# Performance work log

Measured on AMD Instinct MI355X. Metric: run time of the kernel, lower is better.

## Reference

```python
import jax, jax.numpy as jnp
import numpy as np

MAX_DISTANCE = 50.0


def setup_inputs() -> dict:
    key = jax.random.key(0)
    ks = jax.random.split(key, 12)
    B, N, D = 32, 64, 256
    ID = 128  # interaction_dim
    IN = 2 * D + 4  # 516
    H = 2 * ID  # 256
    s = lambda fan_in: 1.0 / np.sqrt(fan_in)
    return {
        "slots": jax.random.normal(ks[0], (B, N, D), jnp.float32),
        "positions": jax.random.normal(ks[1], (B, N, 4), jnp.float32),
        "existence_mask": jnp.ones((B, N), jnp.float32),
        "W1": jax.random.uniform(ks[2], (IN, H), jnp.float32, -s(IN), s(IN)),
        "b1": jax.random.uniform(ks[3], (H,), jnp.float32, -s(IN), s(IN)),
        "W2": jax.random.uniform(ks[4], (H, ID), jnp.float32, -s(H), s(H)),
        "b2": jax.random.uniform(ks[5], (ID,), jnp.float32, -s(H), s(H)),
        "Wt": jax.random.uniform(ks[6], (ID, 8), jnp.float32, -s(ID), s(ID)),
        "bt": jax.random.uniform(ks[7], (8,), jnp.float32, -s(ID), s(ID)),
        "Wc": jax.random.uniform(ks[8], (ID, 1), jnp.float32, -s(ID), s(ID)),
        "bc": jax.random.uniform(ks[9], (1,), jnp.float32, -s(ID), s(ID)),
    }


def reference(slots, positions, existence_mask, W1, b1, W2, b2, Wt, bt, Wc, bc):
    B, N, D = slots.shape
    # all-pairs broadcast of slots: [B, N, N, D]
    slots_i = jnp.broadcast_to(slots[:, :, None, :], (B, N, N, D))
    slots_j = jnp.broadcast_to(slots[:, None, :, :], (B, N, N, D))
    # relative xy position and distance  [B, N, N, 2] / [B, N, N, 1]
    rel_pos = positions[:, :, None, :2] - positions[:, None, :, :2]
    d2 = jnp.sum(rel_pos * rel_pos, axis=-1, keepdims=True)
    safe = jnp.where(d2 == 0, 1.0, d2)
    distance = jnp.where(d2 == 0, 0.0, jnp.sqrt(safe))  # zero-safe norm (matches torch subgradient)
    dn = distance / MAX_DISTANCE
    pair = jnp.concatenate(
        [slots_i, slots_j, rel_pos, dn, jnp.minimum(dn, 1.0)], axis=-1
    )  # [B, N, N, 2D+4]
    h = jax.nn.relu(jnp.einsum("bijf,fh->bijh", pair, W1) + b1)
    feats = jnp.einsum("bijh,hd->bijd", h, W2) + b2  # [B, N, N, ID]
    mask = existence_mask[:, :, None] * existence_mask[:, None, :]  # [B, N, N]
    feats = feats * mask[..., None]
    itypes = jnp.einsum("bijd,dk->bijk", feats, Wt) + bt  # [B, N, N, 8]
    causal = jax.nn.sigmoid(
        (jnp.einsum("bijd,dk->bijk", feats, Wc) + bc)[..., 0]
    ) * mask  # [B, N, N]
    return feats, itypes, causal
```

## Files before the change

kernel.cpp:

```cpp
#include <hip/hip_runtime.h>
#include <hip/hip_bf16.h>
#include <math.h>


typedef __attribute__((ext_vector_type(8))) short  bfrag8;
typedef __attribute__((ext_vector_type(4))) short  spack4;
typedef __attribute__((ext_vector_type(4))) float  fvec4;

#define ITY_OFF   16777216u
#define CAU_OFF   17825792u

static __device__ __forceinline__ short f2bf(float f) {
  unsigned u = __float_as_uint(f);
  u = u + 0x7FFF + ((u >> 16) & 1);
  return (short)(u >> 16);
}
static __device__ __forceinline__ float bf2f(short s) {
  return __uint_as_float(((unsigned)(unsigned short)s) << 16);
}

__global__ __launch_bounds__(256) void prep_wtx(
    const float* __restrict__ W2,
    const float* __restrict__ b2,
    const float* __restrict__ Wt,
    const float* __restrict__ Wc,
    float* __restrict__ Wtx,
    float* __restrict__ b2e)
{
  __shared__ float colv[128];
  __shared__ float red[4];
  const int q   = blockIdx.x;
  const int tid = threadIdx.x;
  if (tid < 128) colv[tid] = (q < 8) ? Wt[tid * 8 + q] : Wc[tid];
  __syncthreads();

  float acc = 0.f;
  #pragma unroll 4
  for (int c = 0; c < 128; ++c)
    acc = fmaf(W2[tid * 128 + c], colv[c], acc);
  Wtx[tid * 16 + q] = acc;

  float p = (tid < 128) ? b2[tid] * colv[tid] : 0.f;
  #pragma unroll
  for (int m = 1; m < 64; m <<= 1) p += __shfl_xor(p, m, 64);
  if ((tid & 63) == 0) red[tid >> 6] = p;
  __syncthreads();
  if (tid == 0) b2e[128 + q] = red[0] + red[1] + red[2] + red[3];
  if (q == 0) {
    if (tid < 128) b2e[tid] = b2[tid];
    if (tid >= 137 && tid < 144) b2e[tid] = 0.f;
  }
}

__global__ __launch_bounds__(256) void prep_w(
    const float* __restrict__ W2,
    const float* __restrict__ Wtx,
    short* __restrict__ WfHi,
    short* __restrict__ WfLo)
{
  const int tid  = threadIdx.x;
  const int tile = blockIdx.x * 4 + (tid >> 6);
  const int l    = tid & 63;
  const int ks   = tile / 9, db = tile - ks * 9;
  const int d    = db * 16 + (l & 15);
  const int k0   = ks * 32 + ((l >> 4) & 3) * 8;

  float v[8];
  if (d < 128) {
    #pragma unroll
    for (int e = 0; e < 8; ++e) v[e] = W2[(k0 + e) * 128 + d];
  } else if (d < 137) {
    #pragma unroll
    for (int e = 0; e < 8; ++e) v[e] = Wtx[(k0 + e) * 16 + (d - 128)];
  } else {
    #pragma unroll
    for (int e = 0; e < 8; ++e) v[e] = 0.f;
  }

  bfrag8 hi, lo;
  #pragma unroll
  for (int e = 0; e < 8; ++e) {
    const short hb = f2bf(v[e]);
    hi[e] = hb;
    lo[e] = f2bf(v[e] - bf2f(hb));
  }
  *(bfrag8*)&WfHi[(tile * 64 + l) * 8] = hi;
  *(bfrag8*)&WfLo[(tile * 64 + l) * 8] = lo;
}

__global__ __launch_bounds__(512) void prep_ac(
    const float* __restrict__ slots,
    const float* __restrict__ W1,
    const float* __restrict__ b1,
    float* __restrict__ Abuf,
    float* __restrict__ Cbuf)
{
  __shared__ __align__(16) float s[4][256];
  __shared__ float pA[4][256], pC[4][256];
  const int tid  = threadIdx.x;
  const int col  = tid & 255;
  const int kh   = tid >> 8;
  const int row0 = blockIdx.x * 4;
  {
    const int r = tid >> 7, o = (tid & 127) * 2;
    *(float2*)&s[r][o] = *(const float2*)&slots[(row0 + r) * 256 + o];
  }
  __syncthreads();

  float aA[4] = {0.f,0.f,0.f,0.f};
  float aC[4] = {0.f,0.f,0.f,0.f};
  const int kbase = kh * 128;
  #pragma unroll 2
  for (int kk = 0; kk < 128; ++kk) {
    const int k = kbase + kk;
    const float wa = W1[k * 256 + col];
    const float wc = W1[(256 + k) * 256 + col];
    #pragma unroll
    for (int r = 0; r < 4; ++r) {
      aA[r] = fmaf(s[r][k], wa, aA[r]);
      aC[r] = fmaf(s[r][k], wc, aC[r]);
    }
  }
  if (kh == 1) {
    #pragma unroll
    for (int r = 0; r < 4; ++r) { pA[r][col] = aA[r]; pC[r][col] = aC[r]; }
  }
  __syncthreads();
  if (kh == 0) {
    const float bv = b1[col];
    #pragma unroll
    for (int r = 0; r < 4; ++r) {
      Abuf[(row0 + r) * 256 + col] = aA[r] + pA[r][col] + bv;
      Cbuf[(row0 + r) * 256 + col] = aC[r] + pC[r][col];
    }
  }
}

__global__ __launch_bounds__(256, 4) void main_kernel(
    const float* __restrict__ positions,
    const float* __restrict__ em,
    const float* __restrict__ W1,
    const float* __restrict__ Abuf,
    const float* __restrict__ Cbuf,
    const float* __restrict__ b2e,
    const short* __restrict__ WfHi,
    const short* __restrict__ WfLo,
    const float* __restrict__ bt,
    const float* __restrict__ bc,
    float* __restrict__ out)
{
  __shared__ __align__(16) char LDSbuf[32768];
  __shared__ float maskL[32];

  const int tid = threadIdx.x;
  const int l   = tid & 63;
  const int w   = tid >> 6;
  const int wid   = (blockIdx.x & 7) * 512 + (blockIdx.x >> 3);
  const int b     = wid >> 7;
  const int i     = (wid >> 1) & 63;
  const int jhalf = wid & 1;
  const int rowi  = b * 64 + i;
  const int j0    = jhalf * 32;

  if (tid < 32) maskL[tid] = em[rowi] * em[b * 64 + j0 + tid];

  char* HhiB = LDSbuf;
  char* HloB = LDSbuf + 16384;

  {
    const int jsub = l >> 4;
    const int kl4  = (l & 15) * 4;
    const float pxi = positions[rowi * 4 + 0];
    const float pyi = positions[rowi * 4 + 1];
    float grx[2], gry[2], gdn[2], gdc[2];
    #pragma unroll
    for (int jj = 0; jj < 2; ++jj) {
      const int rowj = b * 64 + j0 + w * 8 + jsub * 2 + jj;
      const float rx = pxi - positions[rowj * 4 + 0];
      const float ry = pyi - positions[rowj * 4 + 1];
      const float d2 = rx * rx + ry * ry;
      const float dist = (d2 == 0.f) ? 0.f : sqrtf(d2);
      const float dn = dist * (1.0f / 50.0f);
      grx[jj] = rx; gry[jj] = ry; gdn[jj] = dn; gdc[jj] = fminf(dn, 1.f);
    }
    #pragma unroll 1
    for (int kb = 0; kb < 4; ++kb) {
      const int k = kb * 64 + kl4;
      const fvec4 a4 = *(const fvec4*)&Abuf[rowi * 256 + k];
      const fvec4 g0 = *(const fvec4*)&W1[512 * 256 + k];
      const fvec4 g1 = *(const fvec4*)&W1[513 * 256 + k];
      const fvec4 g2 = *(const fvec4*)&W1[514 * 256 + k];
      const fvec4 g3 = *(const fvec4*)&W1[515 * 256 + k];
      #pragma unroll
      for (int jj = 0; jj < 2; ++jj) {
        const int j = w * 8 + jsub * 2 + jj;
        const fvec4 c4 = *(const fvec4*)&Cbuf[(b * 64 + j0 + j) * 256 + k];
        spack4 hi, lo;
        #pragma unroll
        for (int e = 0; e < 4; ++e) {
          float h = a4[e] + c4[e] + grx[jj] * g0[e] + gry[jj] * g1[e]
                  + gdn[jj] * g2[e] + gdc[jj] * g3[e];
          h = fmaxf(h, 0.f);
          const short hb = f2bf(h);
          hi[e] = hb;
          lo[e] = f2bf(h - bf2f(hb));
        }
        const int byte = (j * 512 + k * 2) ^ ((j & 7) << 4);
        *(spack4*)(HhiB + byte) = hi;
        *(spack4*)(HloB + byte) = lo;
      }
    }
  }
  __syncthreads();

  const int laneJ = l & 15;
  const int laneK = l >> 4;
  const int addrA = laneJ * 512 + laneK * 16;
  const int swzA  = (laneJ & 7) << 4;

  fvec4 acc[2][2];
  fvec4 acc8;
  acc[0][0] = 0.f; acc[0][1] = 0.f; acc[1][0] = 0.f; acc[1][1] = 0.f;
  acc8 = 0.f;

  const int db0 = 2 * w, db1 = 2 * w + 1;
  const bool has8 = (w >= 2);
  const int jb8 = w - 2;

  #pragma unroll
  for (int ks = 0; ks < 8; ++ks) {
    const bfrag8 bh0 = *(const bfrag8*)&WfHi[((ks * 9 + db0) * 64 + l) * 8];
    const bfrag8 bl0 = *(const bfrag8*)&WfLo[((ks * 9 + db0) * 64 + l) * 8];
    const bfrag8 bh1 = *(const bfrag8*)&WfHi[((ks * 9 + db1) * 64 + l) * 8];
    const bfrag8 bl1 = *(const bfrag8*)&WfLo[((ks * 9 + db1) * 64 + l) * 8];
    bfrag8 bh8 = {}, bl8 = {};
    if (has8) {
      bh8 = *(const bfrag8*)&WfHi[((ks * 9 + 8) * 64 + l) * 8];
      bl8 = *(const bfrag8*)&WfLo[((ks * 9 + 8) * 64 + l) * 8];
    }
    #pragma unroll
    for (int jb = 0; jb < 2; ++jb) {
      const int base = addrA + jb * 8192 + ks * 64;
      const bfrag8 ah = *(const bfrag8*)(HhiB + (base ^ swzA));
      const bfrag8 al = *(const bfrag8*)(HloB + (base ^ swzA));
      acc[jb][0] = __builtin_amdgcn_mfma_f32_16x16x32_bf16(ah, bh0, acc[jb][0], 0, 0, 0);
      acc[jb][0] = __builtin_amdgcn_mfma_f32_16x16x32_bf16(ah, bl0, acc[jb][0], 0, 0, 0);
      acc[jb][0] = __builtin_amdgcn_mfma_f32_16x16x32_bf16(al, bh0, acc[jb][0], 0, 0, 0);
      acc[jb][1] = __builtin_amdgcn_mfma_f32_16x16x32_bf16(ah, bh1, acc[jb][1], 0, 0, 0);
      acc[jb][1] = __builtin_amdgcn_mfma_f32_16x16x32_bf16(ah, bl1, acc[jb][1], 0, 0, 0);
      acc[jb][1] = __builtin_amdgcn_mfma_f32_16x16x32_bf16(al, bh1, acc[jb][1], 0, 0, 0);
      if (has8 && jb == jb8) {
        acc8 = __builtin_amdgcn_mfma_f32_16x16x32_bf16(ah, bh8, acc8, 0, 0, 0);
        acc8 = __builtin_amdgcn_mfma_f32_16x16x32_bf16(ah, bl8, acc8, 0, 0, 0);
        acc8 = __builtin_amdgcn_mfma_f32_16x16x32_bf16(al, bh8, acc8, 0, 0, 0);
      }
    }
  }

  __syncthreads();

  float* FS = (float*)LDSbuf;
  #pragma unroll
  for (int t = 0; t < 2; ++t) {
    const int d = (2 * w + t) * 16 + laneJ;
    const float bv = b2e[d];
    #pragma unroll
    for (int jb = 0; jb < 2; ++jb) {
      #pragma unroll
      for (int r = 0; r < 4; ++r) {
        const int j = jb * 16 + laneK * 4 + r;
        FS[j * 148 + d] = (acc[jb][t][r] + bv) * maskL[j];
      }
    }
  }
  if (has8) {
    const int d8 = 128 + laneJ;
    const float bv = b2e[d8];
    #pragma unroll
    for (int r = 0; r < 4; ++r) {
      const int j = jb8 * 16 + laneK * 4 + r;
      FS[j * 148 + d8] = (acc8[r] + bv) * maskL[j];
    }
  }
  __syncthreads();

  {
    const int j  = tid >> 3;
    const int dq = (tid & 7) * 16;
    const size_t orow = ((size_t)rowi * 64 + j0 + j) * 128;
    #pragma unroll
    for (int q = 0; q < 4; ++q) {
      const fvec4 v = *(const fvec4*)&FS[j * 148 + dq + q * 4];
      *(fvec4*)&out[orow + dq + q * 4] = v;
    }
    const int q8 = tid & 7;
    out[(size_t)ITY_OFF + ((size_t)rowi * 64 + j0 + j) * 8 + q8] =
        FS[j * 148 + 128 + q8] + bt[q8];
    if (tid < 32) {
      const float z = FS[tid * 148 + 136] + bc[0];
      out[(size_t)CAU_OFF + (size_t)rowi * 64 + j0 + tid] =
          maskL[tid] / (1.f + expf(-z));
    }
  }
}

extern "C" void kernel_launch(void* const* d_in, const int* in_sizes, int n_in,
                              void* d_out, int out_size, void* d_ws, size_t ws_size,
                              hipStream_t stream) {
  const float* slots     = (const float*)d_in[0];
  const float* positions = (const float*)d_in[1];
  const float* em        = (const float*)d_in[2];
  const float* W1        = (const float*)d_in[3];
  const float* b1        = (const float*)d_in[4];
  const float* W2        = (const float*)d_in[5];
  const float* b2        = (const float*)d_in[6];
  const float* Wt        = (const float*)d_in[7];
  const float* bt        = (const float*)d_in[8];
  const float* Wc        = (const float*)d_in[9];
  const float* bc        = (const float*)d_in[10];
  float* out = (float*)d_out;

  float* Abuf = (float*)d_ws;
  float* Cbuf = Abuf + 524288;
  float* b2e  = Cbuf + 524288;
  float* Wtx  = b2e + 256;
  short* WfHi = (short*)(Wtx + 4096);
  short* WfLo = WfHi + 36864;

  prep_wtx<<<9,   256, 0, stream>>>(W2, b2, Wt, Wc, Wtx, b2e);
  prep_w  <<<18,  256, 0, stream>>>(W2, Wtx, WfHi, WfLo);
  prep_ac <<<512, 512, 0, stream>>>(slots, W1, b1, Abuf, Cbuf);
  main_kernel<<<4096, 256, 0, stream>>>(positions, em, W1, Abuf, Cbuf,
                                        b2e, WfHi, WfLo, bt, bc, out);
}
```

Before: 173.3 us.

## Process four full i-rows per block with register-resident W2 fragments

Each block now covers a batch and a group of four i rows, with all 64 j values per row, instead of one half-row. The W2 MFMA B-fragments for each wave's two output tiles are loaded into registers once and reused across the four rows, and the grid shrinks from 4096 to 512 blocks. LDS doubles to 64 KB and the occupancy hint drops to 2 blocks per CU. The intent is to cut redundant weight loads and per-block overhead, at the cost of higher register pressure, serialized per-row phases, and fewer blocks to hide latency.

```diff
diff --git a/kernel.cpp b/kernel.cpp
--- a/kernel.cpp
+++ b/kernel.cpp
@@ -136,7 +136,7 @@
   }
 }
 
-__global__ __launch_bounds__(256, 4) void main_kernel(
+__global__ __launch_bounds__(256, 2) void main_kernel(
     const float* __restrict__ positions,
     const float* __restrict__ em,
     const float* __restrict__ W1,
@@ -149,158 +149,166 @@
     const float* __restrict__ bc,
     float* __restrict__ out)
 {
-  __shared__ __align__(16) char LDSbuf[32768];
-  __shared__ float maskL[32];
+  __shared__ __align__(16) char LDSbuf[65536];
+  __shared__ float maskL[64];
 
   const int tid = threadIdx.x;
   const int l   = tid & 63;
   const int w   = tid >> 6;
-  const int wid   = (blockIdx.x & 7) * 512 + (blockIdx.x >> 3);
-  const int b     = wid >> 7;
-  const int i     = (wid >> 1) & 63;
-  const int jhalf = wid & 1;
-  const int rowi  = b * 64 + i;
-  const int j0    = jhalf * 32;
-
-  if (tid < 32) maskL[tid] = em[rowi] * em[b * 64 + j0 + tid];
+  const int wid = (blockIdx.x & 7) * 64 + (blockIdx.x >> 3);
+  const int b   = wid >> 4;
+  const int ig  = wid & 15;
+
+  if (tid < 64) maskL[tid] = em[b * 64 + tid];
 
   char* HhiB = LDSbuf;
-  char* HloB = LDSbuf + 16384;
-
-  {
-    const int jsub = l >> 4;
-    const int kl4  = (l & 15) * 4;
-    const float pxi = positions[rowi * 4 + 0];
-    const float pyi = positions[rowi * 4 + 1];
-    float grx[2], gry[2], gdn[2], gdc[2];
-    #pragma unroll
-    for (int jj = 0; jj < 2; ++jj) {
-      const int rowj = b * 64 + j0 + w * 8 + jsub * 2 + jj;
-      const float rx = pxi - positions[rowj * 4 + 0];
-      const float ry = pyi - positions[rowj * 4 + 1];
-      const float d2 = rx * rx + ry * ry;
-      const float dist = (d2 == 0.f) ? 0.f : sqrtf(d2);
-      const float dn = dist * (1.0f / 50.0f);
-      grx[jj] = rx; gry[jj] = ry; gdn[jj] = dn; gdc[jj] = fminf(dn, 1.f);
-    }
-    #pragma unroll 1
-    for (int kb = 0; kb < 4; ++kb) {
-      const int k = kb * 64 + kl4;
-      const fvec4 a4 = *(const fvec4*)&Abuf[rowi * 256 + k];
-      const fvec4 g0 = *(const fvec4*)&W1[512 * 256 + k];
-      const fvec4 g1 = *(const fvec4*)&W1[513 * 256 + k];
-      const fvec4 g2 = *(const fvec4*)&W1[514 * 256 + k];
-      const fvec4 g3 = *(const fvec4*)&W1[515 * 256 + k];
-      #pragma unroll
-      for (int jj = 0; jj < 2; ++jj) {
-        const int j = w * 8 + jsub * 2 + jj;
-        const fvec4 c4 = *(const fvec4*)&Cbuf[(b * 64 + j0 + j) * 256 + k];
-        spack4 hi, lo;
-        #pragma unroll
-        for (int e = 0; e < 4; ++e) {
-          float h = a4[e] + c4[e] + grx[jj] * g0[e] + gry[jj] * g1[e]
-                  + gdn[jj] * g2[e] + gdc[jj] * g3[e];
-          h = fmaxf(h, 0.f);
-          const short hb = f2bf(h);
-          hi[e] = hb;
-          lo[e] = f2bf(h - bf2f(hb));
-        }
-        const int byte = (j * 512 + k * 2) ^ ((j & 7) << 4);
-        *(spack4*)(HhiB + byte) = hi;
-        *(spack4*)(HloB + byte) = lo;
-      }
-    }
-  }
-  __syncthreads();
+  char* HloB = LDSbuf + 32768;
+
+  bfrag8 rbh0[8], rbl0[8], rbh1[8], rbl1[8];
+  #pragma unroll
+  for (int ks = 0; ks < 8; ++ks) {
+    rbh0[ks] = *(const bfrag8*)&WfHi[((ks * 9 + 2 * w    ) * 64 + l) * 8];
+    rbl0[ks] = *(const bfrag8*)&WfLo[((ks * 9 + 2 * w    ) * 64 + l) * 8];
+    rbh1[ks] = *(const bfrag8*)&WfHi[((ks * 9 + 2 * w + 1) * 64 + l) * 8];
+    rbl1[ks] = *(const bfrag8*)&WfLo[((ks * 9 + 2 * w + 1) * 64 + l) * 8];
+  }
 
   const int laneJ = l & 15;
   const int laneK = l >> 4;
   const int addrA = laneJ * 512 + laneK * 16;
   const int swzA  = (laneJ & 7) << 4;
 
-  fvec4 acc[2][2];
-  fvec4 acc8;
-  acc[0][0] = 0.f; acc[0][1] = 0.f; acc[1][0] = 0.f; acc[1][1] = 0.f;
-  acc8 = 0.f;
-
-  const int db0 = 2 * w, db1 = 2 * w + 1;
-  const bool has8 = (w >= 2);
-  const int jb8 = w - 2;
-
-  #pragma unroll
-  for (int ks = 0; ks < 8; ++ks) {
-    const bfrag8 bh0 = *(const bfrag8*)&WfHi[((ks * 9 + db0) * 64 + l) * 8];
-    const bfrag8 bl0 = *(const bfrag8*)&WfLo[((ks * 9 + db0) * 64 + l) * 8];
-    const bfrag8 bh1 = *(const bfrag8*)&WfHi[((ks * 9 + db1) * 64 + l) * 8];
-    const bfrag8 bl1 = *(const bfrag8*)&WfLo[((ks * 9 + db1) * 64 + l) * 8];
-    bfrag8 bh8 = {}, bl8 = {};
-    if (has8) {
-      bh8 = *(const bfrag8*)&WfHi[((ks * 9 + 8) * 64 + l) * 8];
-      bl8 = *(const bfrag8*)&WfLo[((ks * 9 + 8) * 64 + l) * 8];
-    }
-    #pragma unroll
-    for (int jb = 0; jb < 2; ++jb) {
-      const int base = addrA + jb * 8192 + ks * 64;
-      const bfrag8 ah = *(const bfrag8*)(HhiB + (base ^ swzA));
-      const bfrag8 al = *(const bfrag8*)(HloB + (base ^ swzA));
-      acc[jb][0] = __builtin_amdgcn_mfma_f32_16x16x32_bf16(ah, bh0, acc[jb][0], 0, 0, 0);
-      acc[jb][0] = __builtin_amdgcn_mfma_f32_16x16x32_bf16(ah, bl0, acc[jb][0], 0, 0, 0);
-      acc[jb][0] = __builtin_amdgcn_mfma_f32_16x16x32_bf16(al, bh0, acc[jb][0], 0, 0, 0);
-      acc[jb][1] = __builtin_amdgcn_mfma_f32_16x16x32_bf16(ah, bh1, acc[jb][1], 0, 0, 0);
-      acc[jb][1] = __builtin_amdgcn_mfma_f32_16x16x32_bf16(ah, bl1, acc[jb][1], 0, 0, 0);
-      acc[jb][1] = __builtin_amdgcn_mfma_f32_16x16x32_bf16(al, bh1, acc[jb][1], 0, 0, 0);
-      if (has8 && jb == jb8) {
-        acc8 = __builtin_amdgcn_mfma_f32_16x16x32_bf16(ah, bh8, acc8, 0, 0, 0);
-        acc8 = __builtin_amdgcn_mfma_f32_16x16x32_bf16(ah, bl8, acc8, 0, 0, 0);
-        acc8 = __builtin_amdgcn_mfma_f32_16x16x32_bf16(al, bh8, acc8, 0, 0, 0);
-      }
-    }
-  }
-
-  __syncthreads();
-
-  float* FS = (float*)LDSbuf;
-  #pragma unroll
-  for (int t = 0; t < 2; ++t) {
-    const int d = (2 * w + t) * 16 + laneJ;
-    const float bv = b2e[d];
-    #pragma unroll
-    for (int jb = 0; jb < 2; ++jb) {
+  #pragma unroll 1
+  for (int ii = 0; ii < 4; ++ii) {
+    const int rowi = b * 64 + ig * 4 + ii;
+    const float emi = em[rowi];
+
+    {
+      const int jsub = laneK;
+      const float pxi = positions[rowi * 4 + 0];
+      const float pyi = positions[rowi * 4 + 1];
+      float grx[4], gry[4], gdn[4], gdc[4];
+      #pragma unroll
+      for (int jj = 0; jj < 4; ++jj) {
+        const int rowj = b * 64 + w * 16 + jsub * 4 + jj;
+        const float rx = pxi - positions[rowj * 4 + 0];
+        const float ry = pyi - positions[rowj * 4 + 1];
+        const float d2 = rx * rx + ry * ry;
+        const float dist = (d2 == 0.f) ? 0.f : sqrtf(d2);
+        const float dn = dist * (1.0f / 50.0f);
+        grx[jj] = rx; gry[jj] = ry; gdn[jj] = dn; gdc[jj] = fminf(dn, 1.f);
+      }
+      #pragma unroll 1
+      for (int kb = 0; kb < 4; ++kb) {
+        const int k = kb * 64 + laneJ * 4;
+        const fvec4 a4 = *(const fvec4*)&Abuf[rowi * 256 + k];
+        const fvec4 g0 = *(const fvec4*)&W1[512 * 256 + k];
+        const fvec4 g1 = *(const fvec4*)&W1[513 * 256 + k];
+        const fvec4 g2 = *(const fvec4*)&W1[514 * 256 + k];
+        const fvec4 g3 = *(const fvec4*)&W1[515 * 256 + k];
+        #pragma unroll
+        for (int jj = 0; jj < 4; ++jj) {
+          const int j = w * 16 + jsub * 4 + jj;
+          const fvec4 c4 = *(const fvec4*)&Cbuf[(b * 64 + j) * 256 + k];
+          spack4 hi, lo;
+          #pragma unroll
+          for (int e = 0; e < 4; ++e) {
+            float h = a4[e] + c4[e] + grx[jj] * g0[e] + gry[jj] * g1[e]
+                    + gdn[jj] * g2[e] + gdc[jj] * g3[e];
+            h = fmaxf(h, 0.f);
+            const short hb = f2bf(h);
+            hi[e] = hb;
+            lo[e] = f2bf(h - bf2f(hb));
+          }
+          const int byte = (j * 512 + k * 2) ^ ((j & 7) << 4);
+          *(spack4*)(HhiB + byte) = hi;
+          *(spack4*)(HloB + byte) = lo;
+        }
+      }
+    }
+    __syncthreads();
+
+    fvec4 acc0[4], acc1[4], acc8;
+    acc0[0] = 0.f; acc0[1] = 0.f; acc0[2] = 0.f; acc0[3] = 0.f;
+    acc1[0] = 0.f; acc1[1] = 0.f; acc1[2] = 0.f; acc1[3] = 0.f;
+    acc8 = 0.f;
+
+    #pragma unroll
+    for (int ks = 0; ks < 8; ++ks) {
+      const bfrag8 bh8 = *(const bfrag8*)&WfHi[((ks * 9 + 8) * 64 + l) * 8];
+      const bfrag8 bl8 = *(const bfrag8*)&WfLo[((ks * 9 + 8) * 64 + l) * 8];
+      #pragma unroll
+      for (int jb = 0; jb < 4; ++jb) {
+        const int base = addrA + jb * 8192 + ks * 64;
+        const bfrag8 ah = *(const bfrag8*)(HhiB + (base ^ swzA));
+        const bfrag8 al = *(const bfrag8*)(HloB + (base ^ swzA));
+        acc0[jb] = __builtin_amdgcn_mfma_f32_16x16x32_bf16(ah, rbh0[ks], acc0[jb], 0, 0, 0);
+        acc0[jb] = __builtin_amdgcn_mfma_f32_16x16x32_bf16(ah, rbl0[ks], acc0[jb], 0, 0, 0);
+        acc0[jb] = __builtin_amdgcn_mfma_f32_16x16x32_bf16(al, rbh0[ks], acc0[jb], 0, 0, 0);
+        acc1[jb] = __builtin_amdgcn_mfma_f32_16x16x32_bf16(ah, rbh1[ks], acc1[jb], 0, 0, 0);
+        acc1[jb] = __builtin_amdgcn_mfma_f32_16x16x32_bf16(ah, rbl1[ks], acc1[jb], 0, 0, 0);
+        acc1[jb] = __builtin_amdgcn_mfma_f32_16x16x32_bf16(al, rbh1[ks], acc1[jb], 0, 0, 0);
+        if (jb == w) {
+          acc8 = __builtin_amdgcn_mfma_f32_16x16x32_bf16(ah, bh8, acc8, 0, 0, 0);
+          acc8 = __builtin_amdgcn_mfma_f32_16x16x32_bf16(ah, bl8, acc8, 0, 0, 0);
+          acc8 = __builtin_amdgcn_mfma_f32_16x16x32_bf16(al, bh8, acc8, 0, 0, 0);
+        }
+      }
+    }
+    __syncthreads();
+
+    float* FS = (float*)LDSbuf;
+    {
+      const int d0 = 2 * w * 16 + laneJ;
+      const int d1 = d0 + 16;
+      const float bv0 = b2e[d0];
+      const float bv1 = b2e[d1];
+      #pragma unroll
+      for (int jb = 0; jb < 4; ++jb) {
+        #pragma unroll
+        for (int r = 0; r < 4; ++r) {
+          const int j = jb * 16 + laneK * 4 + r;
+          const float m = emi * maskL[j];
+          FS[j * 148 + d0] = (acc0[jb][r] + bv0) * m;
+          FS[j * 148 + d1] = (acc1[jb][r] + bv1) * m;
+        }
+      }
+      const int d8 = 128 + laneJ;
+      const float bv8 = b2e[d8];
       #pragma unroll
       for (int r = 0; r < 4; ++r) {
-        const int j = jb * 16 + laneK * 4 + r;
-        FS[j * 148 + d] = (acc[jb][t][r] + bv) * maskL[j];
-      }
-    }
-  }
-  if (has8) {
-    const int d8 = 128 + laneJ;
-    const float bv = b2e[d8];
-    #pragma unroll
-    for (int r = 0; r < 4; ++r) {
-      const int j = jb8 * 16 + laneK * 4 + r;
-      FS[j * 148 + d8] = (acc8[r] + bv) * maskL[j];
-    }
-  }
-  __syncthreads();
-
-  {
-    const int j  = tid >> 3;
-    const int dq = (tid & 7) * 16;
-    const size_t orow = ((size_t)rowi * 64 + j0 + j) * 128;
-    #pragma unroll
-    for (int q = 0; q < 4; ++q) {
-      const fvec4 v = *(const fvec4*)&FS[j * 148 + dq + q * 4];
-      *(fvec4*)&out[orow + dq + q * 4] = v;
-    }
-    const int q8 = tid & 7;
-    out[(size_t)ITY_OFF + ((size_t)rowi * 64 + j0 + j) * 8 + q8] =
-        FS[j * 148 + 128 + q8] + bt[q8];
-    if (tid < 32) {
-      const float z = FS[tid * 148 + 136] + bc[0];
-      out[(size_t)CAU_OFF + (size_t)rowi * 64 + j0 + tid] =
-          maskL[tid] / (1.f + expf(-z));
-    }
+        const int j = w * 16 + laneK * 4 + r;
+        FS[j * 148 + d8] = (acc8[r] + bv8) * (emi * maskL[j]);
+      }
+    }
+    __syncthreads();
+
+    {
+      const int j  = tid >> 2;
+      const int dc = (tid & 3) * 32;
+      const size_t orow = ((size_t)rowi * 64 + j) * 128;
+      #pragma unroll
+      for (int q = 0; q < 8; ++q) {
+        const fvec4 v = *(const fvec4*)&FS[j * 148 + dc + q * 4];
+        *(fvec4*)&out[orow + dc + q * 4] = v;
+      }
+    }
+    {
+      const int jq = tid >> 3;
+      const int q8 = tid & 7;
+      #pragma unroll
+      for (int r = 0; r < 2; ++r) {
+        const int j = r * 32 + jq;
+        out[(size_t)ITY_OFF + ((size_t)rowi * 64 + j) * 8 + q8] =
+            FS[j * 148 + 128 + q8] + bt[q8];
+      }
+      if (tid < 64) {
+        const float z = FS[tid * 148 + 136] + bc[0];
+        out[(size_t)CAU_OFF + (size_t)rowi * 64 + tid] =
+            (emi * maskL[tid]) / (1.f + expf(-z));
+      }
+    }
+    __syncthreads();
   }
 }
 
@@ -330,6 +338,6 @@
   prep_wtx<<<9,   256, 0, stream>>>(W2, b2, Wt, Wc, Wtx, b2e);
   prep_w  <<<18,  256, 0, stream>>>(W2, Wtx, WfHi, WfLo);
   prep_ac <<<512, 512, 0, stream>>>(slots, W1, b1, Abuf, Cbuf);
-  main_kernel<<<4096, 256, 0, stream>>>(positions, em, W1, Abuf, Cbuf,
-                                        b2e, WfHi, WfLo, bt, bc, out);
-}
+  main_kernel<<<512, 256, 0, stream>>>(positions, em, W1, Abuf, Cbuf,
+                                       b2e, WfHi, WfLo, bt, bc, out);
+}
```

Result: slower. 237.2 us (+36.9%).
